# Kernel tuning notes

Measured on AMD Instinct MI355X. Metric: run time of the kernel, lower is better.

Reference implementation:

```python
import jax, jax.numpy as jnp
import numpy as np

P = 8192          # pool_size
D = 4096          # input_dim
B = 4             # batch
SPARSITY = 0.1
NC = int(P * P * SPARSITY)  # 6710886 COO nonzeros


def setup_inputs() -> dict:
    key = jax.random.key(0)
    ks = jax.random.split(key, 5)
    return {
        "x": jax.random.normal(ks[0], (B, D), dtype=jnp.float32),
        "W_proj": jax.random.normal(ks[1], (P, D), dtype=jnp.float32) / np.float32(np.sqrt(D)),
        "b_proj": jnp.zeros((P,), dtype=jnp.float32),
        "conn_values": jax.random.normal(ks[2], (NC,), dtype=jnp.float32) * 0.1,
        "sparse_state": jnp.zeros((P,), dtype=jnp.float32),
        "conn_rows": jax.random.randint(ks[3], (NC,), 0, P, dtype=jnp.int32),
        "conn_cols": jax.random.randint(ks[4], (NC,), 0, P, dtype=jnp.int32),
    }


def reference(x, W_proj, b_proj, conn_values, sparse_state, conn_rows, conn_cols):
    # input projection: [B, D] @ [D, P] -> [B, P]
    a = x @ W_proj.T + b_proj
    # quantile threshold over all elements of |a| (matches torch.quantile on full tensor)
    thr = jnp.quantile(jnp.abs(a), 1.0 - SPARSITY)
    mask = jnp.abs(a) > thr                     # [B, P]
    # decay old state, then overwrite active entries with row-0 activation
    a0, m0 = a[0], mask[0]                      # [P], [P]
    state = jnp.where(m0, a0, sparse_state * 0.9)
    # sparse COO matvec: recurrent[r] += v * state[c] for each nonzero (r, c, v)
    contrib = conn_values * state[conn_cols]    # [NC]
    recurrent = jax.ops.segment_sum(contrib, conn_rows, num_segments=P)
    # fused state update + exact GELU (torch nn.GELU default)
    new_state = jax.nn.gelu(state + 0.1 * recurrent, approximate=False)
    # BoundedAttractorState scalars
    active_count = m0.sum()
    mean_activity = jnp.where(
        active_count > 0,
        jnp.sum(jnp.where(m0, new_state, 0.0)) / jnp.maximum(active_count, 1).astype(new_state.dtype),
        0.0,
    )
    return new_state, active_count, mean_activity
```

## Files before the change

### kernel.cpp

```cpp
#include <hip/hip_runtime.h>
#include <math.h>

#define PP 8192
#define DD 4096
#define NTOT 32768
#define K_LOW 29490
#define NBINS 8192
#define SCALE 1048576.0f
#define INV_SCALE (1.0f / 1048576.0f)
#define MSCALE 262144.0f
#define INV_MSCALE (1.0f / 262144.0f)
#define LIST_CAP 3072

__device__ __forceinline__ float dot4(float4 w, float4 v) {
  return fmaf(w.x, v.x, fmaf(w.y, v.y, fmaf(w.z, v.z, w.w * v.w)));
}

__global__ __launch_bounds__(256, 4) void gemm_kernel(const float* __restrict__ x,
                                                      const float* __restrict__ W,
                                                      const float* __restrict__ bias,
                                                      float* __restrict__ a,
                                                      int* __restrict__ rec,
                                                      int* __restrict__ acc) {
  if (blockIdx.x < 32) {
    rec[blockIdx.x * 256 + threadIdx.x] = 0;
  } else if (blockIdx.x == 32 && threadIdx.x < 4) {
    acc[threadIdx.x] = 0;
  }
  const int wave = threadIdx.x >> 6;
  const int lane = threadIdx.x & 63;
  const int p0 = blockIdx.x * 16 + wave * 4;
  const float4* __restrict__ Wr[4];
  #pragma unroll
  for (int r = 0; r < 4; ++r) Wr[r] = (const float4*)(W + (size_t)(p0 + r) * DD);
  const float4* __restrict__ x4 = (const float4*)x;
  double accd[4][4];
  #pragma unroll
  for (int r = 0; r < 4; ++r)
    #pragma unroll
    for (int b = 0; b < 4; ++b) accd[r][b] = 0.0;
  #pragma unroll 2
  for (int k = 0; k < 16; ++k) {
    const int i = lane + k * 64;
    float4 w0 = Wr[0][i];
    float4 w1 = Wr[1][i];
    float4 w2 = Wr[2][i];
    float4 w3 = Wr[3][i];
    float4 v0 = x4[i];
    float4 v1 = x4[1024 + i];
    float4 v2 = x4[2048 + i];
    float4 v3 = x4[3072 + i];
    accd[0][0] += (double)dot4(w0, v0);
    accd[0][1] += (double)dot4(w0, v1);
    accd[0][2] += (double)dot4(w0, v2);
    accd[0][3] += (double)dot4(w0, v3);
    accd[1][0] += (double)dot4(w1, v0);
    accd[1][1] += (double)dot4(w1, v1);
    accd[1][2] += (double)dot4(w1, v2);
    accd[1][3] += (double)dot4(w1, v3);
    accd[2][0] += (double)dot4(w2, v0);
    accd[2][1] += (double)dot4(w2, v1);
    accd[2][2] += (double)dot4(w2, v2);
    accd[2][3] += (double)dot4(w2, v3);
    accd[3][0] += (double)dot4(w3, v0);
    accd[3][1] += (double)dot4(w3, v1);
    accd[3][2] += (double)dot4(w3, v2);
    accd[3][3] += (double)dot4(w3, v3);
  }
  #pragma unroll
  for (int r = 0; r < 4; ++r)
    #pragma unroll
    for (int b = 0; b < 4; ++b)
      #pragma unroll
      for (int off = 32; off > 0; off >>= 1)
        accd[r][b] += __shfl_down(accd[r][b], off);
  if (lane < 4) {
  }
  if (lane == 0) {
    #pragma unroll
    for (int r = 0; r < 4; ++r) {
      float bp = bias[p0 + r];
      #pragma unroll
      for (int b = 0; b < 4; ++b) a[b * PP + p0 + r] = (float)accd[r][b] + bp;
    }
  }
}

__global__ __launch_bounds__(1024) void thr_kernel(const float* __restrict__ a,
                                                   float* __restrict__ thr) {
  __shared__ unsigned h[NBINS];
  __shared__ unsigned scan[1024];
  __shared__ unsigned list1[LIST_CAP];
  __shared__ unsigned list2[LIST_CAP];
  __shared__ unsigned s_n1, s_n2;
  __shared__ unsigned s_b1, s_r1, s_b2, s_r2;
  __shared__ unsigned s_vlo, s_vhi;
  const int tid = threadIdx.x;
  #pragma unroll
  for (int j = 0; j < NBINS / 1024; ++j) h[tid + j * 1024] = 0u;
  if (tid == 0) { s_n1 = 0; s_n2 = 0; }
  __syncthreads();
  for (int i = tid; i < NTOT; i += 1024) {
    unsigned u = __float_as_uint(fabsf(a[i]));
    atomicAdd(&h[u >> 18], 1u);
  }
  __syncthreads();
  unsigned bins[8];
  #pragma unroll
  for (int j = 0; j < 8; ++j) bins[j] = h[tid * 8 + j];
  unsigned part = 0;
  #pragma unroll
  for (int j = 0; j < 8; ++j) part += bins[j];
  scan[tid] = part;
  __syncthreads();
  for (int off = 1; off < 1024; off <<= 1) {
    unsigned v = (tid >= off) ? scan[tid - off] : 0u;
    __syncthreads();
    scan[tid] += v;
    __syncthreads();
  }
  const unsigned incl = scan[tid];
  const unsigned excl = incl - part;
  if (excl <= (unsigned)K_LOW && (unsigned)K_LOW < incl) {
    unsigned r = (unsigned)K_LOW - excl, cum = 0;
    #pragma unroll
    for (int j = 0; j < 8; ++j) {
      if (cum + bins[j] > r) { s_b1 = tid * 8 + j; s_r1 = r - cum; break; }
      cum += bins[j];
    }
  }
  if (excl <= (unsigned)(K_LOW + 1) && (unsigned)(K_LOW + 1) < incl) {
    unsigned r = (unsigned)(K_LOW + 1) - excl, cum = 0;
    #pragma unroll
    for (int j = 0; j < 8; ++j) {
      if (cum + bins[j] > r) { s_b2 = tid * 8 + j; s_r2 = r - cum; break; }
      cum += bins[j];
    }
  }
  __syncthreads();
  const unsigned b1 = s_b1, r1 = s_r1, b2 = s_b2, r2 = s_r2;
  for (int i = tid; i < NTOT; i += 1024) {
    unsigned u = __float_as_uint(fabsf(a[i]));
    unsigned bk = u >> 18;
    if (bk == b1) {
      unsigned idx = atomicAdd(&s_n1, 1u);
      if (idx < LIST_CAP) list1[idx] = u;
    } else if (bk == b2) {
      unsigned idx = atomicAdd(&s_n2, 1u);
      if (idx < LIST_CAP) list2[idx] = u;
    }
  }
  __syncthreads();
  const unsigned m1 = min(s_n1, (unsigned)LIST_CAP);
  const unsigned m2 = min(s_n2, (unsigned)LIST_CAP);
  for (unsigned i = tid; i < m1; i += 1024) {
    unsigned ui = list1[i];
    unsigned ltc = 0, eqb = 0;
    for (unsigned j = 0; j < m1; ++j) {
      unsigned uj = list1[j];
      ltc += (uj < ui) ? 1u : 0u;
      eqb += ((uj == ui) && (j < i)) ? 1u : 0u;
    }
    unsigned rk = ltc + eqb;
    if (rk == r1) s_vlo = ui;
    if (b2 == b1 && rk == r2) s_vhi = ui;
  }
  if (b2 != b1) {
    for (unsigned i = tid; i < m2; i += 1024) {
      unsigned ui = list2[i];
      unsigned ltc = 0, eqb = 0;
      for (unsigned j = 0; j < m2; ++j) {
        unsigned uj = list2[j];
        ltc += (uj < ui) ? 1u : 0u;
        eqb += ((uj == ui) && (j < i)) ? 1u : 0u;
      }
      if (ltc + eqb == r2) s_vhi = ui;
    }
  }
  __syncthreads();
  if (tid == 0) {
    double dlo = (double)__uint_as_float(s_vlo);
    double dhi = (double)__uint_as_float(s_vhi);
    double idx = 0.9 * (double)(NTOT - 1);
    double g = idx - floor(idx);
    thr[0] = (float)(dlo + g * (dhi - dlo));
  }
}

__global__ __launch_bounds__(1024) void spmv_kernel(const float* __restrict__ vals,
                                                    const int* __restrict__ rows,
                                                    const int* __restrict__ cols,
                                                    const float* __restrict__ a,
                                                    const float* __restrict__ thr,
                                                    const float* __restrict__ sstate,
                                                    int* __restrict__ rec,
                                                    int nc) {
  __shared__ float s_state[PP];
  __shared__ int s_rec[PP];
  const int tid = threadIdx.x;
  const float t = thr[0];
  for (int i = tid; i < PP; i += 1024) {
    float a0 = a[i];
    s_state[i] = (fabsf(a0) > t) ? a0 : 0.9f * sstate[i];
    s_rec[i] = 0;
  }
  __syncthreads();
  const int n4 = nc >> 2;
  const int stride = gridDim.x * 1024;
  const float4* __restrict__ v4 = (const float4*)vals;
  const int4* __restrict__ r4 = (const int4*)rows;
  const int4* __restrict__ c4 = (const int4*)cols;
  for (int i = blockIdx.x * 1024 + tid; i < n4; i += stride) {
    float4 v = v4[i];
    int4 r = r4[i];
    int4 c = c4[i];
    atomicAdd((unsigned*)&s_rec[r.x], (unsigned)__float2int_rn(v.x * s_state[c.x] * SCALE));
    atomicAdd((unsigned*)&s_rec[r.y], (unsigned)__float2int_rn(v.y * s_state[c.y] * SCALE));
    atomicAdd((unsigned*)&s_rec[r.z], (unsigned)__float2int_rn(v.z * s_state[c.z] * SCALE));
    atomicAdd((unsigned*)&s_rec[r.w], (unsigned)__float2int_rn(v.w * s_state[c.w] * SCALE));
  }
  if (blockIdx.x == 0 && tid < (nc - (n4 << 2))) {
    int i = (n4 << 2) + tid;
    atomicAdd((unsigned*)&s_rec[rows[i]],
              (unsigned)__float2int_rn(vals[i] * s_state[cols[i]] * SCALE));
  }
  __syncthreads();
  for (int i = tid; i < PP; i += 1024)
    atomicAdd((unsigned*)&rec[i], (unsigned)s_rec[i]);
}

__global__ __launch_bounds__(256) void finalize_kernel(const int* __restrict__ rec,
                                                       const float* __restrict__ a,
                                                       const float* __restrict__ thr,
                                                       const float* __restrict__ sstate,
                                                       float* __restrict__ out,
                                                       int* __restrict__ acc) {
  __shared__ float wsum[4];
  __shared__ unsigned wcnt[4];
  const int p = blockIdx.x * 256 + threadIdx.x;
  const float t = thr[0];
  float r = (float)rec[p] * INV_SCALE;
  float a0 = a[p];
  float st = (fabsf(a0) > t) ? a0 : 0.9f * sstate[p];
  float v = st + 0.1f * r;
  float ns = 0.5f * v * (1.0f + erff(v * 0.70710678118654752440f));
  out[p] = ns;
  bool m = fabsf(a0) > t;
  float lsum = m ? ns : 0.0f;
  unsigned lcnt = m ? 1u : 0u;
  #pragma unroll
  for (int off = 32; off > 0; off >>= 1) {
    lsum += __shfl_down(lsum, off);
    lcnt += __shfl_down(lcnt, off);
  }
  const int lane = threadIdx.x & 63;
  const int wid = threadIdx.x >> 6;
  if (lane == 0) { wsum[wid] = lsum; wcnt[wid] = lcnt; }
  __syncthreads();
  if (threadIdx.x == 0) {
    float bsum = wsum[0] + wsum[1] + wsum[2] + wsum[3];
    unsigned bcnt = wcnt[0] + wcnt[1] + wcnt[2] + wcnt[3];
    atomicAdd((unsigned*)&acc[0], (unsigned)__float2int_rn(bsum * MSCALE));
    atomicAdd((unsigned*)&acc[1], bcnt);
    __threadfence();
    unsigned d = atomicAdd((unsigned*)&acc[2], 1u);
    if (d == (unsigned)(gridDim.x - 1)) {
      int sfix = atomicAdd(&acc[0], 0);
      int cnt = atomicAdd(&acc[1], 0);
      out[PP] = (float)cnt;
      out[PP + 1] = (cnt > 0) ? ((float)sfix * INV_MSCALE / (float)cnt) : 0.0f;
    }
  }
}

extern "C" void kernel_launch(void* const* d_in, const int* in_sizes, int n_in,
                              void* d_out, int out_size, void* d_ws, size_t ws_size,
                              hipStream_t stream) {
  const float* x      = (const float*)d_in[0];
  const float* W      = (const float*)d_in[1];
  const float* bias   = (const float*)d_in[2];
  const float* vals   = (const float*)d_in[3];
  const float* sstate = (const float*)d_in[4];
  const int*   rows   = (const int*)d_in[5];
  const int*   cols   = (const int*)d_in[6];
  const int    nc     = in_sizes[3];
  float* out = (float*)d_out;
  float* ws  = (float*)d_ws;

  float* a   = ws;
  float* thr = ws + 32768;
  int*   rec = (int*)(ws + 32784);
  int*   acc = (int*)(ws + 32784 + PP);

  gemm_kernel<<<PP / 16, 256, 0, stream>>>(x, W, bias, a, rec, acc);
  thr_kernel<<<1, 1024, 0, stream>>>(a, thr);
  spmv_kernel<<<256, 1024, 0, stream>>>(vals, rows, cols, a, thr, sstate, rec, nc);
  finalize_kernel<<<PP / 256, 256, 0, stream>>>(rec, a, thr, sstate, out, acc);
}
```

Before: 85.06 us.

## Fuse GEMM, quantile, SpMV and finalize into one persistent kernel with grid barriers

```diff
diff --git a/kernel.cpp b/kernel.cpp
--- a/kernel.cpp
+++ b/kernel.cpp
@@ -11,265 +11,288 @@
 #define MSCALE 262144.0f
 #define INV_MSCALE (1.0f / 262144.0f)
 #define LIST_CAP 3072
+#define NBLK 256
+#define NTHR 512
 
 __device__ __forceinline__ float dot4(float4 w, float4 v) {
   return fmaf(w.x, v.x, fmaf(w.y, v.y, fmaf(w.z, v.z, w.w * v.w)));
 }
 
-__global__ __launch_bounds__(256, 4) void gemm_kernel(const float* __restrict__ x,
-                                                      const float* __restrict__ W,
-                                                      const float* __restrict__ bias,
-                                                      float* __restrict__ a,
-                                                      int* __restrict__ rec,
-                                                      int* __restrict__ acc) {
-  if (blockIdx.x < 32) {
-    rec[blockIdx.x * 256 + threadIdx.x] = 0;
-  } else if (blockIdx.x == 32 && threadIdx.x < 4) {
-    acc[threadIdx.x] = 0;
-  }
-  const int wave = threadIdx.x >> 6;
-  const int lane = threadIdx.x & 63;
-  const int p0 = blockIdx.x * 16 + wave * 4;
-  const float4* __restrict__ Wr[4];
-  #pragma unroll
-  for (int r = 0; r < 4; ++r) Wr[r] = (const float4*)(W + (size_t)(p0 + r) * DD);
-  const float4* __restrict__ x4 = (const float4*)x;
-  double accd[4][4];
-  #pragma unroll
-  for (int r = 0; r < 4; ++r)
+struct ThrShared {
+  unsigned h[NBINS];
+  unsigned list1[LIST_CAP];
+  unsigned list2[LIST_CAP];
+  unsigned scan[NTHR];
+  unsigned n1, n2, b1, r1, b2, r2, vlo, vhi;
+};
+struct SpmvShared {
+  float st[PP];
+  int   rc[PP];
+};
+union FusedShared {
+  ThrShared t;
+  SpmvShared s;
+};
+
+__device__ __forceinline__ void grid_barrier(unsigned* cnt, unsigned target) {
+  __threadfence();
+  __syncthreads();
+  if (threadIdx.x == 0) {
+    atomicAdd(cnt, 1u);
+    while (atomicAdd(cnt, 0u) < target) __builtin_amdgcn_s_sleep(2);
+  }
+  __syncthreads();
+  __threadfence();
+}
+
+__global__ __launch_bounds__(NTHR) void fused_kernel(
+    const float* __restrict__ x, const float* __restrict__ W,
+    const float* __restrict__ bias, const float* __restrict__ vals,
+    const int* __restrict__ rows, const int* __restrict__ cols,
+    const float* __restrict__ sstate, float* __restrict__ a,
+    int* __restrict__ rec, int* __restrict__ acc, unsigned* __restrict__ bar,
+    float* __restrict__ out, int nc) {
+  __shared__ FusedShared sh;
+  const int tid = threadIdx.x;
+  const int blk = blockIdx.x;
+  const int lane = tid & 63;
+  const int wave = tid >> 6;
+
+  {
+    const int g = blk * NTHR + tid;
+    if (g < PP) rec[g] = 0;
+    if (g >= PP && g < PP + 4) acc[g - PP] = 0;
+  }
+
+  {
+    const int p0 = blk * 32 + wave * 4;
+    const float4* __restrict__ Wr0 = (const float4*)(W + (size_t)p0 * DD);
+    const float4* __restrict__ Wr1 = (const float4*)(W + (size_t)(p0 + 1) * DD);
+    const float4* __restrict__ Wr2 = (const float4*)(W + (size_t)(p0 + 2) * DD);
+    const float4* __restrict__ Wr3 = (const float4*)(W + (size_t)(p0 + 3) * DD);
+    const float4* __restrict__ x4 = (const float4*)x;
+    double accd[4][4];
     #pragma unroll
-    for (int b = 0; b < 4; ++b) accd[r][b] = 0.0;
-  #pragma unroll 2
-  for (int k = 0; k < 16; ++k) {
-    const int i = lane + k * 64;
-    float4 w0 = Wr[0][i];
-    float4 w1 = Wr[1][i];
-    float4 w2 = Wr[2][i];
-    float4 w3 = Wr[3][i];
-    float4 v0 = x4[i];
-    float4 v1 = x4[1024 + i];
-    float4 v2 = x4[2048 + i];
-    float4 v3 = x4[3072 + i];
-    accd[0][0] += (double)dot4(w0, v0);
-    accd[0][1] += (double)dot4(w0, v1);
-    accd[0][2] += (double)dot4(w0, v2);
-    accd[0][3] += (double)dot4(w0, v3);
-    accd[1][0] += (double)dot4(w1, v0);
-    accd[1][1] += (double)dot4(w1, v1);
-    accd[1][2] += (double)dot4(w1, v2);
-    accd[1][3] += (double)dot4(w1, v3);
-    accd[2][0] += (double)dot4(w2, v0);
-    accd[2][1] += (double)dot4(w2, v1);
-    accd[2][2] += (double)dot4(w2, v2);
-    accd[2][3] += (double)dot4(w2, v3);
-    accd[3][0] += (double)dot4(w3, v0);
-    accd[3][1] += (double)dot4(w3, v1);
-    accd[3][2] += (double)dot4(w3, v2);
-    accd[3][3] += (double)dot4(w3, v3);
-  }
-  #pragma unroll
-  for (int r = 0; r < 4; ++r)
+    for (int r = 0; r < 4; ++r)
+      #pragma unroll
+      for (int b = 0; b < 4; ++b) accd[r][b] = 0.0;
+    #pragma unroll 2
+    for (int k = 0; k < 16; ++k) {
+      const int i = lane + k * 64;
+      float4 w0 = Wr0[i];
+      float4 w1 = Wr1[i];
+      float4 w2 = Wr2[i];
+      float4 w3 = Wr3[i];
+      float4 v0 = x4[i];
+      float4 v1 = x4[1024 + i];
+      float4 v2 = x4[2048 + i];
+      float4 v3 = x4[3072 + i];
+      accd[0][0] += (double)dot4(w0, v0);
+      accd[0][1] += (double)dot4(w0, v1);
+      accd[0][2] += (double)dot4(w0, v2);
+      accd[0][3] += (double)dot4(w0, v3);
+      accd[1][0] += (double)dot4(w1, v0);
+      accd[1][1] += (double)dot4(w1, v1);
+      accd[1][2] += (double)dot4(w1, v2);
+      accd[1][3] += (double)dot4(w1, v3);
+      accd[2][0] += (double)dot4(w2, v0);
+      accd[2][1] += (double)dot4(w2, v1);
+      accd[2][2] += (double)dot4(w2, v2);
+      accd[2][3] += (double)dot4(w2, v3);
+      accd[3][0] += (double)dot4(w3, v0);
+      accd[3][1] += (double)dot4(w3, v1);
+      accd[3][2] += (double)dot4(w3, v2);
+      accd[3][3] += (double)dot4(w3, v3);
+    }
     #pragma unroll
-    for (int b = 0; b < 4; ++b)
-      #pragma unroll
-      for (int off = 32; off > 0; off >>= 1)
-        accd[r][b] += __shfl_down(accd[r][b], off);
-  if (lane < 4) {
-  }
-  if (lane == 0) {
+    for (int r = 0; r < 4; ++r)
+      #pragma unroll
+      for (int b = 0; b < 4; ++b)
+        #pragma unroll
+        for (int off = 32; off > 0; off >>= 1)
+          accd[r][b] += __shfl_down(accd[r][b], off);
+    if (lane == 0) {
+      #pragma unroll
+      for (int r = 0; r < 4; ++r) {
+        float bp = bias[p0 + r];
+        #pragma unroll
+        for (int b = 0; b < 4; ++b) a[b * PP + p0 + r] = (float)accd[r][b] + bp;
+      }
+    }
+  }
+
+  const int quads = nc >> 2;
+  const int per = (quads + NBLK - 1) / NBLK;
+  const int lo = blk * per;
+  const int hi = min(lo + per, quads);
+  {
+    const float4* __restrict__ v4 = (const float4*)vals;
+    const int4* __restrict__ r4 = (const int4*)rows;
+    const int4* __restrict__ c4 = (const int4*)cols;
+    float fs = 0.0f;
+    int is = 0;
+    for (int i = lo + tid; i < hi; i += NTHR) {
+      float4 v = v4[i];
+      int4 r = r4[i];
+      int4 c = c4[i];
+      fs += v.x + v.y + v.z + v.w;
+      is += r.x + r.y + r.z + r.w + c.x + c.y + c.z + c.w;
+    }
+    asm volatile("" :: "v"(fs), "v"(is));
+  }
+
+  grid_barrier(bar, NBLK);
+
+  float thr_v;
+  {
+    for (int j = tid; j < NBINS; j += NTHR) sh.t.h[j] = 0u;
+    if (tid == 0) { sh.t.n1 = 0; sh.t.n2 = 0; }
+    __syncthreads();
+    for (int i = tid; i < NTOT; i += NTHR)
+      atomicAdd(&sh.t.h[__float_as_uint(fabsf(a[i])) >> 18], 1u);
+    __syncthreads();
+    unsigned bins[16];
+    unsigned part = 0;
     #pragma unroll
-    for (int r = 0; r < 4; ++r) {
-      float bp = bias[p0 + r];
-      #pragma unroll
-      for (int b = 0; b < 4; ++b) a[b * PP + p0 + r] = (float)accd[r][b] + bp;
-    }
-  }
-}
-
-__global__ __launch_bounds__(1024) void thr_kernel(const float* __restrict__ a,
-                                                   float* __restrict__ thr) {
-  __shared__ unsigned h[NBINS];
-  __shared__ unsigned scan[1024];
-  __shared__ unsigned list1[LIST_CAP];
-  __shared__ unsigned list2[LIST_CAP];
-  __shared__ unsigned s_n1, s_n2;
-  __shared__ unsigned s_b1, s_r1, s_b2, s_r2;
-  __shared__ unsigned s_vlo, s_vhi;
-  const int tid = threadIdx.x;
-  #pragma unroll
-  for (int j = 0; j < NBINS / 1024; ++j) h[tid + j * 1024] = 0u;
-  if (tid == 0) { s_n1 = 0; s_n2 = 0; }
-  __syncthreads();
-  for (int i = tid; i < NTOT; i += 1024) {
-    unsigned u = __float_as_uint(fabsf(a[i]));
-    atomicAdd(&h[u >> 18], 1u);
-  }
-  __syncthreads();
-  unsigned bins[8];
-  #pragma unroll
-  for (int j = 0; j < 8; ++j) bins[j] = h[tid * 8 + j];
-  unsigned part = 0;
-  #pragma unroll
-  for (int j = 0; j < 8; ++j) part += bins[j];
-  scan[tid] = part;
-  __syncthreads();
-  for (int off = 1; off < 1024; off <<= 1) {
-    unsigned v = (tid >= off) ? scan[tid - off] : 0u;
-    __syncthreads();
-    scan[tid] += v;
-    __syncthreads();
-  }
-  const unsigned incl = scan[tid];
-  const unsigned excl = incl - part;
-  if (excl <= (unsigned)K_LOW && (unsigned)K_LOW < incl) {
-    unsigned r = (unsigned)K_LOW - excl, cum = 0;
-    #pragma unroll
-    for (int j = 0; j < 8; ++j) {
-      if (cum + bins[j] > r) { s_b1 = tid * 8 + j; s_r1 = r - cum; break; }
-      cum += bins[j];
-    }
-  }
-  if (excl <= (unsigned)(K_LOW + 1) && (unsigned)(K_LOW + 1) < incl) {
-    unsigned r = (unsigned)(K_LOW + 1) - excl, cum = 0;
-    #pragma unroll
-    for (int j = 0; j < 8; ++j) {
-      if (cum + bins[j] > r) { s_b2 = tid * 8 + j; s_r2 = r - cum; break; }
-      cum += bins[j];
-    }
-  }
-  __syncthreads();
-  const unsigned b1 = s_b1, r1 = s_r1, b2 = s_b2, r2 = s_r2;
-  for (int i = tid; i < NTOT; i += 1024) {
-    unsigned u = __float_as_uint(fabsf(a[i]));
-    unsigned bk = u >> 18;
-    if (bk == b1) {
-      unsigned idx = atomicAdd(&s_n1, 1u);
-      if (idx < LIST_CAP) list1[idx] = u;
-    } else if (bk == b2) {
-      unsigned idx = atomicAdd(&s_n2, 1u);
-      if (idx < LIST_CAP) list2[idx] = u;
-    }
-  }
-  __syncthreads();
-  const unsigned m1 = min(s_n1, (unsigned)LIST_CAP);
-  const unsigned m2 = min(s_n2, (unsigned)LIST_CAP);
-  for (unsigned i = tid; i < m1; i += 1024) {
-    unsigned ui = list1[i];
-    unsigned ltc = 0, eqb = 0;
-    for (unsigned j = 0; j < m1; ++j) {
-      unsigned uj = list1[j];
-      ltc += (uj < ui) ? 1u : 0u;
-      eqb += ((uj == ui) && (j < i)) ? 1u : 0u;
-    }
-    unsigned rk = ltc + eqb;
-    if (rk == r1) s_vlo = ui;
-    if (b2 == b1 && rk == r2) s_vhi = ui;
-  }
-  if (b2 != b1) {
-    for (unsigned i = tid; i < m2; i += 1024) {
-      unsigned ui = list2[i];
+    for (int j = 0; j < 16; ++j) {
+      bins[j] = sh.t.h[tid * 16 + j];
+      part += bins[j];
+    }
+    sh.t.scan[tid] = part;
+    __syncthreads();
+    for (int off = 1; off < NTHR; off <<= 1) {
+      unsigned vv = (tid >= off) ? sh.t.scan[tid - off] : 0u;
+      __syncthreads();
+      sh.t.scan[tid] += vv;
+      __syncthreads();
+    }
+    const unsigned incl = sh.t.scan[tid];
+    const unsigned excl = incl - part;
+    if (excl <= (unsigned)K_LOW && (unsigned)K_LOW < incl) {
+      unsigned r = (unsigned)K_LOW - excl, cum = 0;
+      #pragma unroll
+      for (int j = 0; j < 16; ++j) {
+        if (cum + bins[j] > r) { sh.t.b1 = tid * 16 + j; sh.t.r1 = r - cum; break; }
+        cum += bins[j];
+      }
+    }
+    if (excl <= (unsigned)(K_LOW + 1) && (unsigned)(K_LOW + 1) < incl) {
+      unsigned r = (unsigned)(K_LOW + 1) - excl, cum = 0;
+      #pragma unroll
+      for (int j = 0; j < 16; ++j) {
+        if (cum + bins[j] > r) { sh.t.b2 = tid * 16 + j; sh.t.r2 = r - cum; break; }
+        cum += bins[j];
+      }
+    }
+    __syncthreads();
+    const unsigned b1 = sh.t.b1, r1 = sh.t.r1, b2 = sh.t.b2, r2 = sh.t.r2;
+    for (int i = tid; i < NTOT; i += NTHR) {
+      unsigned u = __float_as_uint(fabsf(a[i]));
+      unsigned bk = u >> 18;
+      if (bk == b1) {
+        unsigned idx = atomicAdd(&sh.t.n1, 1u);
+        if (idx < LIST_CAP) sh.t.list1[idx] = u;
+      } else if (bk == b2) {
+        unsigned idx = atomicAdd(&sh.t.n2, 1u);
+        if (idx < LIST_CAP) sh.t.list2[idx] = u;
+      }
+    }
+    __syncthreads();
+    const unsigned m1 = min(sh.t.n1, (unsigned)LIST_CAP);
+    const unsigned m2 = min(sh.t.n2, (unsigned)LIST_CAP);
+    for (unsigned i = tid; i < m1; i += NTHR) {
+      unsigned ui = sh.t.list1[i];
       unsigned ltc = 0, eqb = 0;
-      for (unsigned j = 0; j < m2; ++j) {
-        unsigned uj = list2[j];
+      for (unsigned j = 0; j < m1; ++j) {
+        unsigned uj = sh.t.list1[j];
         ltc += (uj < ui) ? 1u : 0u;
         eqb += ((uj == ui) && (j < i)) ? 1u : 0u;
       }
-      if (ltc + eqb == r2) s_vhi = ui;
-    }
-  }
-  __syncthreads();
-  if (tid == 0) {
-    double dlo = (double)__uint_as_float(s_vlo);
-    double dhi = (double)__uint_as_float(s_vhi);
-    double idx = 0.9 * (double)(NTOT - 1);
-    double g = idx - floor(idx);
-    thr[0] = (float)(dlo + g * (dhi - dlo));
-  }
-}
-
-__global__ __launch_bounds__(1024) void spmv_kernel(const float* __restrict__ vals,
-                                                    const int* __restrict__ rows,
-                                                    const int* __restrict__ cols,
-                                                    const float* __restrict__ a,
-                                                    const float* __restrict__ thr,
-                                                    const float* __restrict__ sstate,
-                                                    int* __restrict__ rec,
-                                                    int nc) {
-  __shared__ float s_state[PP];
-  __shared__ int s_rec[PP];
-  const int tid = threadIdx.x;
-  const float t = thr[0];
-  for (int i = tid; i < PP; i += 1024) {
-    float a0 = a[i];
-    s_state[i] = (fabsf(a0) > t) ? a0 : 0.9f * sstate[i];
-    s_rec[i] = 0;
-  }
-  __syncthreads();
-  const int n4 = nc >> 2;
-  const int stride = gridDim.x * 1024;
-  const float4* __restrict__ v4 = (const float4*)vals;
-  const int4* __restrict__ r4 = (const int4*)rows;
-  const int4* __restrict__ c4 = (const int4*)cols;
-  for (int i = blockIdx.x * 1024 + tid; i < n4; i += stride) {
-    float4 v = v4[i];
-    int4 r = r4[i];
-    int4 c = c4[i];
-    atomicAdd((unsigned*)&s_rec[r.x], (unsigned)__float2int_rn(v.x * s_state[c.x] * SCALE));
-    atomicAdd((unsigned*)&s_rec[r.y], (unsigned)__float2int_rn(v.y * s_state[c.y] * SCALE));
-    atomicAdd((unsigned*)&s_rec[r.z], (unsigned)__float2int_rn(v.z * s_state[c.z] * SCALE));
-    atomicAdd((unsigned*)&s_rec[r.w], (unsigned)__float2int_rn(v.w * s_state[c.w] * SCALE));
-  }
-  if (blockIdx.x == 0 && tid < (nc - (n4 << 2))) {
-    int i = (n4 << 2) + tid;
-    atomicAdd((unsigned*)&s_rec[rows[i]],
-              (unsigned)__float2int_rn(vals[i] * s_state[cols[i]] * SCALE));
-  }
-  __syncthreads();
-  for (int i = tid; i < PP; i += 1024)
-    atomicAdd((unsigned*)&rec[i], (unsigned)s_rec[i]);
-}
-
-__global__ __launch_bounds__(256) void finalize_kernel(const int* __restrict__ rec,
-                                                       const float* __restrict__ a,
-                                                       const float* __restrict__ thr,
-                                                       const float* __restrict__ sstate,
-                                                       float* __restrict__ out,
-                                                       int* __restrict__ acc) {
-  __shared__ float wsum[4];
-  __shared__ unsigned wcnt[4];
-  const int p = blockIdx.x * 256 + threadIdx.x;
-  const float t = thr[0];
-  float r = (float)rec[p] * INV_SCALE;
-  float a0 = a[p];
-  float st = (fabsf(a0) > t) ? a0 : 0.9f * sstate[p];
-  float v = st + 0.1f * r;
-  float ns = 0.5f * v * (1.0f + erff(v * 0.70710678118654752440f));
-  out[p] = ns;
-  bool m = fabsf(a0) > t;
-  float lsum = m ? ns : 0.0f;
-  unsigned lcnt = m ? 1u : 0u;
-  #pragma unroll
-  for (int off = 32; off > 0; off >>= 1) {
-    lsum += __shfl_down(lsum, off);
-    lcnt += __shfl_down(lcnt, off);
-  }
-  const int lane = threadIdx.x & 63;
-  const int wid = threadIdx.x >> 6;
-  if (lane == 0) { wsum[wid] = lsum; wcnt[wid] = lcnt; }
-  __syncthreads();
-  if (threadIdx.x == 0) {
-    float bsum = wsum[0] + wsum[1] + wsum[2] + wsum[3];
-    unsigned bcnt = wcnt[0] + wcnt[1] + wcnt[2] + wcnt[3];
-    atomicAdd((unsigned*)&acc[0], (unsigned)__float2int_rn(bsum * MSCALE));
-    atomicAdd((unsigned*)&acc[1], bcnt);
-    __threadfence();
-    unsigned d = atomicAdd((unsigned*)&acc[2], 1u);
-    if (d == (unsigned)(gridDim.x - 1)) {
-      int sfix = atomicAdd(&acc[0], 0);
-      int cnt = atomicAdd(&acc[1], 0);
-      out[PP] = (float)cnt;
-      out[PP + 1] = (cnt > 0) ? ((float)sfix * INV_MSCALE / (float)cnt) : 0.0f;
-    }
+      unsigned rk = ltc + eqb;
+      if (rk == r1) sh.t.vlo = ui;
+      if (b2 == b1 && rk == r2) sh.t.vhi = ui;
+    }
+    if (b2 != b1) {
+      for (unsigned i = tid; i < m2; i += NTHR) {
+        unsigned ui = sh.t.list2[i];
+        unsigned ltc = 0, eqb = 0;
+        for (unsigned j = 0; j < m2; ++j) {
+          unsigned uj = sh.t.list2[j];
+          ltc += (uj < ui) ? 1u : 0u;
+          eqb += ((uj == ui) && (j < i)) ? 1u : 0u;
+        }
+        if (ltc + eqb == r2) sh.t.vhi = ui;
+      }
+    }
+    __syncthreads();
+    const double dlo = (double)__uint_as_float(sh.t.vlo);
+    const double dhi = (double)__uint_as_float(sh.t.vhi);
+    const double idxq = 0.9 * (double)(NTOT - 1);
+    const double gq = idxq - floor(idxq);
+    thr_v = (float)(dlo + gq * (dhi - dlo));
+    __syncthreads();
+  }
+
+  {
+    for (int i = tid; i < PP; i += NTHR) {
+      float a0 = a[i];
+      sh.s.st[i] = (fabsf(a0) > thr_v) ? a0 : 0.9f * sstate[i];
+      sh.s.rc[i] = 0;
+    }
+    __syncthreads();
+    const float4* __restrict__ v4 = (const float4*)vals;
+    const int4* __restrict__ r4 = (const int4*)rows;
+    const int4* __restrict__ c4 = (const int4*)cols;
+    for (int i = lo + tid; i < hi; i += NTHR) {
+      float4 v = v4[i];
+      int4 r = r4[i];
+      int4 c = c4[i];
+      atomicAdd((unsigned*)&sh.s.rc[r.x], (unsigned)__float2int_rn(v.x * sh.s.st[c.x] * SCALE));
+      atomicAdd((unsigned*)&sh.s.rc[r.y], (unsigned)__float2int_rn(v.y * sh.s.st[c.y] * SCALE));
+      atomicAdd((unsigned*)&sh.s.rc[r.z], (unsigned)__float2int_rn(v.z * sh.s.st[c.z] * SCALE));
+      atomicAdd((unsigned*)&sh.s.rc[r.w], (unsigned)__float2int_rn(v.w * sh.s.st[c.w] * SCALE));
+    }
+    if (blk == 0 && tid < (nc - (quads << 2))) {
+      int i = (quads << 2) + tid;
+      atomicAdd((unsigned*)&sh.s.rc[rows[i]],
+                (unsigned)__float2int_rn(vals[i] * sh.s.st[cols[i]] * SCALE));
+    }
+    __syncthreads();
+    for (int i = tid; i < PP; i += NTHR)
+      atomicAdd((unsigned*)&rec[i], (unsigned)sh.s.rc[i]);
+  }
+
+  grid_barrier(bar, 2u * NBLK);
+
+  if (blk < 16) {
+    const int p = blk * NTHR + tid;
+    float r = (float)rec[p] * INV_SCALE;
+    float a0 = a[p];
+    bool m = fabsf(a0) > thr_v;
+    float st = m ? a0 : 0.9f * sstate[p];
+    float v = st + 0.1f * r;
+    float ns = 0.5f * v * (1.0f + erff(v * 0.70710678118654752440f));
+    out[p] = ns;
+    float lsum = m ? ns : 0.0f;
+    unsigned lcnt = m ? 1u : 0u;
+    #pragma unroll
+    for (int off = 32; off > 0; off >>= 1) {
+      lsum += __shfl_down(lsum, off);
+      lcnt += __shfl_down(lcnt, off);
+    }
+    if (lane == 0) {
+      atomicAdd((unsigned*)&acc[0], (unsigned)__float2int_rn(lsum * MSCALE));
+      atomicAdd((unsigned*)&acc[1], lcnt);
+    }
+  }
+
+  grid_barrier(bar, 3u * NBLK);
+
+  if (blk == 0 && tid == 0) {
+    int sfix = (int)atomicAdd((unsigned*)&acc[0], 0u);
+    int cnt = (int)atomicAdd((unsigned*)&acc[1], 0u);
+    out[PP] = (float)cnt;
+    out[PP + 1] = (cnt > 0) ? ((float)sfix * INV_MSCALE / (float)cnt) : 0.0f;
   }
 }
 
@@ -287,13 +310,12 @@
   float* out = (float*)d_out;
   float* ws  = (float*)d_ws;
 
-  float* a   = ws;
-  float* thr = ws + 32768;
-  int*   rec = (int*)(ws + 32784);
-  int*   acc = (int*)(ws + 32784 + PP);
-
-  gemm_kernel<<<PP / 16, 256, 0, stream>>>(x, W, bias, a, rec, acc);
-  thr_kernel<<<1, 1024, 0, stream>>>(a, thr);
-  spmv_kernel<<<256, 1024, 0, stream>>>(vals, rows, cols, a, thr, sstate, rec, nc);
-  finalize_kernel<<<PP / 256, 256, 0, stream>>>(rec, a, thr, sstate, out, acc);
+  float*    a   = ws;
+  int*      rec = (int*)(ws + 32768);
+  int*      acc = (int*)(ws + 32768 + PP);
+  unsigned* bar = (unsigned*)(ws + 32768 + PP + 4);
+
+  hipMemsetAsync(bar, 0, 4 * sizeof(unsigned), stream);
+  fused_kernel<<<NBLK, NTHR, 0, stream>>>(x, W, bias, vals, rows, cols, sstate,
+                                          a, rec, acc, bar, out, nc);
 }
```

Result: slower. 335.1 us (+294.0%).
